# Optimization experiments

Measured on AMD Instinct MI355X. Metric: run time of the kernel, lower is better.

Reference implementation:

```python
import jax, jax.numpy as jnp
import numpy as np

D = 256; H = 8; DFFN = 512; L = 3; P = 4
SHAPES = [(64, 64), (32, 32), (16, 16)]  # (Hl, Wl) per level
LQ = 64 * 64
LV = sum(h * w for h, w in SHAPES)
B = 1


def _ln(x, g, b):
    m = x.mean(-1, keepdims=True)
    v = ((x - m) ** 2).mean(-1, keepdims=True)
    return (x - m) / jnp.sqrt(v + 1e-5) * g + b


def _mha(q, k, v, Wi, bi, Wo, bo):
    Dh = D // H
    B_, Lq, _ = q.shape
    qp = (q @ Wi[:D].T + bi[:D]).reshape(B_, Lq, H, Dh)
    kp = (k @ Wi[D:2 * D].T + bi[D:2 * D]).reshape(B_, -1, H, Dh)
    vp = (v @ Wi[2 * D:].T + bi[2 * D:]).reshape(B_, -1, H, Dh)
    s = jnp.einsum('bqhd,bkhd->bhqk', qp, kp) / jnp.sqrt(jnp.asarray(Dh, qp.dtype))
    a = jax.nn.softmax(s, axis=-1)
    o = jnp.einsum('bhqk,bkhd->bqhd', a, vp).reshape(B_, Lq, D)
    return o @ Wo.T + bo


def _msdeform(q, ref, value_in, off_w, off_b, attn_w, attn_b, val_w, val_b, out_w, out_b):
    B_, Lq, _ = q.shape
    Dh = D // H
    value = (value_in @ val_w.T + val_b).reshape(B_, LV, H, Dh)
    off = (q @ off_w.T + off_b).reshape(B_, Lq, H, L, P, 2)
    aw = jax.nn.softmax((q @ attn_w.T + attn_b).reshape(B_, Lq, H, L * P), axis=-1)
    aw = aw.reshape(B_, Lq, H, L, P)
    norm = jnp.asarray([[w, h] for h, w in SHAPES], dtype=q.dtype)  # (W,H) per level
    loc = ref[:, :, None, :, None, :] + off / norm[None, None, None, :, None, :]
    out = jnp.zeros((B_, H, Lq, Dh), q.dtype)
    start = 0
    for l, (Hl, Wl) in enumerate(SHAPES):
        v = value[:, start:start + Hl * Wl].transpose(0, 2, 1, 3)  # [B,H,Hl*Wl,Dh]
        start += Hl * Wl
        # grid_sample align_corners=False, padding_mode='zeros'
        x = loc[:, :, :, l, :, 0] * Wl - 0.5  # [B,Lq,H,P]
        y = loc[:, :, :, l, :, 1] * Hl - 0.5
        x0 = jnp.floor(x); y0 = jnp.floor(y)
        wx = x - x0; wy = y - y0
        x0i = x0.astype(jnp.int32); y0i = y0.astype(jnp.int32)

        def gather(xi, yi):
            valid = ((xi >= 0) & (xi < Wl) & (yi >= 0) & (yi < Hl)).astype(q.dtype)
            idx = jnp.clip(yi, 0, Hl - 1) * Wl + jnp.clip(xi, 0, Wl - 1)
            idx = idx.transpose(0, 2, 1, 3).reshape(B_, H, Lq * P, 1)
            g = jnp.take_along_axis(v, idx, axis=2)  # [B,H,Lq*P,Dh]
            return g * valid.transpose(0, 2, 1, 3).reshape(B_, H, Lq * P, 1)

        g00 = gather(x0i, y0i); g01 = gather(x0i + 1, y0i)
        g10 = gather(x0i, y0i + 1); g11 = gather(x0i + 1, y0i + 1)

        def r(t):
            return t.transpose(0, 2, 1, 3).reshape(B_, H, Lq * P, 1)

        wxr = r(wx); wyr = r(wy)
        samp = (g00 * (1 - wxr) * (1 - wyr) + g01 * wxr * (1 - wyr)
                + g10 * (1 - wxr) * wyr + g11 * wxr * wyr)
        a = r(aw[:, :, :, l])
        out = out + (samp * a).reshape(B_, H, Lq, P, Dh).sum(axis=3)
    o = out.transpose(0, 2, 1, 3).reshape(B_, Lq, D)
    return o @ out_w.T + out_b


def _forward(bev_queries, img_feats_flat, ref_points, bev_pos,
             mha_in_w, mha_in_b, mha_out_w, mha_out_b, norm1_g, norm1_b,
             off_w, off_b, attn_w, attn_b, val_w, val_b, ca_out_w, ca_out_b,
             norm2_g, norm2_b, ffn_w1, ffn_b1, ffn_w2, ffn_b2, ffn_g, ffn_bb):
    q = bev_queries + bev_pos
    x = _ln(bev_queries + _mha(q, q, bev_queries, mha_in_w, mha_in_b, mha_out_w, mha_out_b),
            norm1_g, norm1_b)
    q2 = x + bev_pos
    x = _ln(x + _msdeform(q2, ref_points, img_feats_flat, off_w, off_b, attn_w, attn_b,
                          val_w, val_b, ca_out_w, ca_out_b), norm2_g, norm2_b)
    h = jax.nn.relu(x @ ffn_w1.T + ffn_b1) @ ffn_w2.T + ffn_b2
    return _ln(x + h, ffn_g, ffn_bb)


def setup_inputs() -> dict:
    key = jax.random.key(0)
    ks = jax.random.split(key, 16)
    f = jax.random.normal
    return {
        'bev_queries': f(ks[0], (B, LQ, D), jnp.float32),
        'img_feats_flat': f(ks[1], (B, LV, D), jnp.float32),
        'ref_points': jax.random.uniform(ks[2], (B, LQ, L, 2), jnp.float32),
        'spatial_shapes': jnp.asarray(SHAPES, dtype=jnp.int32),
        'bev_pos': f(ks[3], (B, LQ, D), jnp.float32),
        'mha_in_w': f(ks[4], (3 * D, D)) * 0.02, 'mha_in_b': jnp.zeros((3 * D,)),
        'mha_out_w': f(ks[5], (D, D)) * 0.02, 'mha_out_b': jnp.zeros((D,)),
        'norm1_g': jnp.ones((D,)), 'norm1_b': jnp.zeros((D,)),
        'off_w': f(ks[6], (H * L * P * 2, D)) * 0.02,
        'off_b': jax.random.uniform(ks[7], (H * L * P * 2,), minval=-2.0, maxval=2.0),
        'attn_w': f(ks[8], (H * L * P, D)) * 0.02, 'attn_b': jnp.zeros((H * L * P,)),
        'val_w': f(ks[9], (D, D)) * 0.02, 'val_b': jnp.zeros((D,)),
        'ca_out_w': f(ks[10], (D, D)) * 0.02, 'ca_out_b': jnp.zeros((D,)),
        'norm2_g': jnp.ones((D,)), 'norm2_b': jnp.zeros((D,)),
        'ffn_w1': f(ks[11], (DFFN, D)) * 0.02, 'ffn_b1': jnp.zeros((DFFN,)),
        'ffn_w2': f(ks[12], (D, DFFN)) * 0.02, 'ffn_b2': jnp.zeros((D,)),
        'ffn_g': jnp.ones((D,)), 'ffn_bb': jnp.zeros((D,)),
    }


def reference(bev_queries, img_feats_flat, ref_points, spatial_shapes, bev_pos,
              mha_in_w, mha_in_b, mha_out_w, mha_out_b, norm1_g, norm1_b,
              off_w, off_b, attn_w, attn_b, val_w, val_b, ca_out_w, ca_out_b,
              norm2_g, norm2_b, ffn_w1, ffn_b1, ffn_w2, ffn_b2, ffn_g, ffn_bb):
    del spatial_shapes  # static; baked into SHAPES
    return _forward(bev_queries, img_feats_flat, ref_points, bev_pos,
                    mha_in_w, mha_in_b, mha_out_w, mha_out_b, norm1_g, norm1_b,
                    off_w, off_b, attn_w, attn_b, val_w, val_b, ca_out_w, ca_out_b,
                    norm2_g, norm2_b, ffn_w1, ffn_b1, ffn_w2, ffn_b2, ffn_g, ffn_bb)
```

## Files before the change

kernel.cpp:

```cpp
#include <hip/hip_runtime.h>
#include <math.h>


#define LQ_N 4096
#define LV_N 5376

typedef short short8 __attribute__((ext_vector_type(8)));
typedef float f32x4 __attribute__((ext_vector_type(4)));

__device__ inline unsigned short f2b(float f) {
  union { float f; unsigned u; } v;
  v.f = f;
  return (unsigned short)((v.u + 0x7FFFu + ((v.u >> 16) & 1u)) >> 16);
}

__device__ __forceinline__ void gemm_body(
    const float* __restrict__ A, const float* __restrict__ A2,
    const float* __restrict__ W, const float* __restrict__ bias,
    float* __restrict__ C, int M, int N, int K, int relu, int bm, int bn) {
  __shared__ unsigned short Asb[64][40];
  __shared__ unsigned short Wsb[64][40];
  const int tid = threadIdx.x;
  const int w = tid >> 6, lane = tid & 63;
  const int g = lane >> 4, li = lane & 15;
  f32x4 acc[4] = {{0.f, 0.f, 0.f, 0.f}, {0.f, 0.f, 0.f, 0.f},
                  {0.f, 0.f, 0.f, 0.f}, {0.f, 0.f, 0.f, 0.f}};
  for (int k0 = 0; k0 < K; k0 += 32) {
    __syncthreads();
#pragma unroll
    for (int i = 0; i < 2; ++i) {
      int r = (tid >> 3) + i * 32;
      int c = (tid & 7) * 4;
      int gr = bm + r;
      float4 av = make_float4(0.f, 0.f, 0.f, 0.f);
      if (gr < M) {
        av = *reinterpret_cast<const float4*>(&A[(size_t)gr * K + k0 + c]);
        if (A2) {
          float4 bv = *reinterpret_cast<const float4*>(&A2[(size_t)gr * K + k0 + c]);
          av.x += bv.x; av.y += bv.y; av.z += bv.z; av.w += bv.w;
        }
      }
      Asb[r][c + 0] = f2b(av.x); Asb[r][c + 1] = f2b(av.y);
      Asb[r][c + 2] = f2b(av.z); Asb[r][c + 3] = f2b(av.w);
      int gw = bn + r;
      float4 wv = make_float4(0.f, 0.f, 0.f, 0.f);
      if (gw < N) wv = *reinterpret_cast<const float4*>(&W[(size_t)gw * K + k0 + c]);
      Wsb[r][c + 0] = f2b(wv.x); Wsb[r][c + 1] = f2b(wv.y);
      Wsb[r][c + 2] = f2b(wv.z); Wsb[r][c + 3] = f2b(wv.w);
    }
    __syncthreads();
    short8 af = *reinterpret_cast<const short8*>(&Asb[w * 16 + li][g * 8]);
#pragma unroll
    for (int nt = 0; nt < 4; ++nt) {
      short8 wf = *reinterpret_cast<const short8*>(&Wsb[nt * 16 + li][g * 8]);
      acc[nt] = __builtin_amdgcn_mfma_f32_16x16x32_bf16(af, wf, acc[nt], 0, 0, 0);
    }
  }
#pragma unroll
  for (int nt = 0; nt < 4; ++nt) {
#pragma unroll
    for (int reg = 0; reg < 4; ++reg) {
      int row = bm + w * 16 + g * 4 + reg;
      int col = bn + nt * 16 + li;
      if (row < M && col < N) {
        float v = acc[nt][reg] + bias[col];
        if (relu) v = fmaxf(v, 0.f);
        C[(size_t)row * N + col] = v;
      }
    }
  }
}

__global__ __launch_bounds__(256) void gemm_bf16_kernel(
    const float* __restrict__ A, const float* __restrict__ A2,
    const float* __restrict__ W, const float* __restrict__ bias,
    float* __restrict__ C, int M, int N, int K, int relu) {
  gemm_body(A, A2, W, bias, C, M, N, K, relu, blockIdx.y * 64, blockIdx.x * 64);
}

__global__ __launch_bounds__(256) void qkv_kernel(
    const float* __restrict__ bevq, const float* __restrict__ bevpos,
    const float* __restrict__ w, const float* __restrict__ b,
    float* __restrict__ out) {
  const int z = blockIdx.z;
  gemm_body(bevq, z < 2 ? bevpos : nullptr, w + (size_t)z * 256 * 256, b + z * 256,
            out + (size_t)z * 1048576, LQ_N, 256, 256, 0,
            blockIdx.y * 64, blockIdx.x * 64);
}

__global__ __launch_bounds__(256) void attn_mfma_kernel(
    const float* __restrict__ qp, const float* __restrict__ kp,
    const float* __restrict__ vp, float* __restrict__ out) {
  const int h = blockIdx.y;
  const int q0 = blockIdx.x * 64;
  __shared__ unsigned short Qsb[64][40];
  __shared__ unsigned short Ksb[64][40];
  __shared__ unsigned short Vtb[32][72];
  __shared__ unsigned short Plds[4][16][72];
  const int tid = threadIdx.x;
  const int w = tid >> 6, lane = tid & 63;
  const int g = lane >> 4, li = lane & 15;
  const float scale = 0.17677669529663687f;

#pragma unroll
  for (int i = 0; i < 2; ++i) {
    int r = (tid >> 3) + i * 32;
    int c = (tid & 7) * 4;
    float4 v = *reinterpret_cast<const float4*>(&qp[(size_t)(q0 + r) * 256 + h * 32 + c]);
    Qsb[r][c + 0] = f2b(v.x * scale); Qsb[r][c + 1] = f2b(v.y * scale);
    Qsb[r][c + 2] = f2b(v.z * scale); Qsb[r][c + 3] = f2b(v.w * scale);
  }
  __syncthreads();
  short8 qfrag = *reinterpret_cast<const short8*>(&Qsb[w * 16 + li][g * 8]);

  f32x4 oacc[2] = {{0.f, 0.f, 0.f, 0.f}, {0.f, 0.f, 0.f, 0.f}};
  float m_run[4] = {-1e30f, -1e30f, -1e30f, -1e30f};
  float l_run[4] = {0.f, 0.f, 0.f, 0.f};

  for (int kt = 0; kt < LQ_N; kt += 64) {
    __syncthreads();
#pragma unroll
    for (int i = 0; i < 2; ++i) {
      int r = (tid >> 3) + i * 32;
      int c = (tid & 7) * 4;
      float4 kv = *reinterpret_cast<const float4*>(&kp[(size_t)(kt + r) * 256 + h * 32 + c]);
      Ksb[r][c + 0] = f2b(kv.x); Ksb[r][c + 1] = f2b(kv.y);
      Ksb[r][c + 2] = f2b(kv.z); Ksb[r][c + 3] = f2b(kv.w);
      float4 vv = *reinterpret_cast<const float4*>(&vp[(size_t)(kt + r) * 256 + h * 32 + c]);
      Vtb[c + 0][r] = f2b(vv.x); Vtb[c + 1][r] = f2b(vv.y);
      Vtb[c + 2][r] = f2b(vv.z); Vtb[c + 3][r] = f2b(vv.w);
    }
    __syncthreads();

    f32x4 s[4];
#pragma unroll
    for (int nt = 0; nt < 4; ++nt) {
      short8 kf = *reinterpret_cast<const short8*>(&Ksb[nt * 16 + li][g * 8]);
      f32x4 z = {0.f, 0.f, 0.f, 0.f};
      s[nt] = __builtin_amdgcn_mfma_f32_16x16x32_bf16(qfrag, kf, z, 0, 0, 0);
    }

#pragma unroll
    for (int reg = 0; reg < 4; ++reg) {
      float m = fmaxf(fmaxf(s[0][reg], s[1][reg]), fmaxf(s[2][reg], s[3][reg]));
      m = fmaxf(m, __shfl_xor(m, 1));
      m = fmaxf(m, __shfl_xor(m, 2));
      m = fmaxf(m, __shfl_xor(m, 4));
      m = fmaxf(m, __shfl_xor(m, 8));
      float mn = fmaxf(m_run[reg], m);
      float corr = __expf(m_run[reg] - mn);
      m_run[reg] = mn;
      float ls = 0.f;
#pragma unroll
      for (int nt = 0; nt < 4; ++nt) {
        float p = __expf(s[nt][reg] - mn);
        s[nt][reg] = p;
        ls += p;
      }
      ls += __shfl_xor(ls, 1);
      ls += __shfl_xor(ls, 2);
      ls += __shfl_xor(ls, 4);
      ls += __shfl_xor(ls, 8);
      l_run[reg] = l_run[reg] * corr + ls;
#pragma unroll
      for (int nt = 0; nt < 4; ++nt)
        Plds[w][g * 4 + reg][nt * 16 + li] = f2b(s[nt][reg]);
      oacc[0][reg] *= corr;
      oacc[1][reg] *= corr;
    }

#pragma unroll
    for (int ks = 0; ks < 2; ++ks) {
      short8 pf = *reinterpret_cast<const short8*>(&Plds[w][li][ks * 32 + g * 8]);
#pragma unroll
      for (int nt2 = 0; nt2 < 2; ++nt2) {
        short8 vf = *reinterpret_cast<const short8*>(&Vtb[nt2 * 16 + li][ks * 32 + g * 8]);
        oacc[nt2] = __builtin_amdgcn_mfma_f32_16x16x32_bf16(pf, vf, oacc[nt2], 0, 0, 0);
      }
    }
  }

#pragma unroll
  for (int reg = 0; reg < 4; ++reg) {
    float invl = 1.f / l_run[reg];
    int row = q0 + w * 16 + g * 4 + reg;
#pragma unroll
    for (int nt2 = 0; nt2 < 2; ++nt2)
      out[(size_t)row * 256 + h * 32 + nt2 * 16 + li] = oacc[nt2][reg] * invl;
  }
}

__global__ __launch_bounds__(256) void add_ln_kernel(
    const float* __restrict__ a, const float* __restrict__ b,
    const float* __restrict__ g, const float* __restrict__ bb,
    float* __restrict__ out) {
  int row = blockIdx.x, t = threadIdx.x;
  float v = a[(size_t)row * 256 + t] + b[(size_t)row * 256 + t];
  float s = v;
#pragma unroll
  for (int m = 32; m >= 1; m >>= 1) s += __shfl_xor(s, m);
  __shared__ float red[4], red2[4];
  int wave = t >> 6, lane = t & 63;
  if (lane == 0) red[wave] = s;
  __syncthreads();
  float mean = (red[0] + red[1] + red[2] + red[3]) * (1.f / 256.f);
  float dv = v - mean;
  float s2 = dv * dv;
#pragma unroll
  for (int m = 32; m >= 1; m >>= 1) s2 += __shfl_xor(s2, m);
  if (lane == 0) red2[wave] = s2;
  __syncthreads();
  float var = (red2[0] + red2[1] + red2[2] + red2[3]) * (1.f / 256.f);
  out[(size_t)row * 256 + t] = dv * rsqrtf(var + 1e-5f) * g[t] + bb[t];
}

__global__ __launch_bounds__(256) void msdeform_kernel(
    const float* __restrict__ value,
    const float* __restrict__ off,
    const float* __restrict__ awl,
    const float* __restrict__ ref,
    float* __restrict__ out) {
  int qi = blockIdx.x;
  int tid = threadIdx.x;
  int h = tid >> 5, d = tid & 31;
  float w[12];
  float mx = -1e30f;
#pragma unroll
  for (int j = 0; j < 12; ++j) {
    w[j] = awl[(size_t)qi * 96 + h * 12 + j];
    mx = fmaxf(mx, w[j]);
  }
  float ssum = 0.f;
#pragma unroll
  for (int j = 0; j < 12; ++j) {
    w[j] = __expf(w[j] - mx);
    ssum += w[j];
  }
  float inv = 1.f / ssum;
  const int starts[3] = {0, 4096, 5120};
  const int dims[3] = {64, 32, 16};
  float acc = 0.f;
#pragma unroll
  for (int l = 0; l < 3; ++l) {
    const int Wl = dims[l], Hl = dims[l];
    float rx = ref[(size_t)qi * 6 + l * 2 + 0];
    float ry = ref[(size_t)qi * 6 + l * 2 + 1];
    auto fetch = [&](int xi, int yi) -> float {
      if (xi < 0 || xi >= Wl || yi < 0 || yi >= Hl) return 0.f;
      return value[(size_t)(starts[l] + yi * Wl + xi) * 256 + h * 32 + d];
    };
#pragma unroll
    for (int p = 0; p < 4; ++p) {
      int oidx = qi * 192 + ((h * 3 + l) * 4 + p) * 2;
      float ox = off[oidx], oy = off[oidx + 1];
      float x = (rx + ox / (float)Wl) * (float)Wl - 0.5f;
      float y = (ry + oy / (float)Hl) * (float)Hl - 0.5f;
      float x0f = floorf(x), y0f = floorf(y);
      float wx = x - x0f, wy = y - y0f;
      int x0 = (int)x0f, y0 = (int)y0f;
      float g00 = fetch(x0, y0);
      float g01 = fetch(x0 + 1, y0);
      float g10 = fetch(x0, y0 + 1);
      float g11 = fetch(x0 + 1, y0 + 1);
      float samp = g00 * (1.f - wx) * (1.f - wy) + g01 * wx * (1.f - wy) +
                   g10 * (1.f - wx) * wy + g11 * wx * wy;
      acc += samp * w[l * 4 + p] * inv;
    }
  }
  out[(size_t)qi * 256 + h * 32 + d] = acc;
}

extern "C" void kernel_launch(void* const* d_in, const int* in_sizes, int n_in,
                              void* d_out, int out_size, void* d_ws, size_t ws_size,
                              hipStream_t stream) {
  const float* bevq   = (const float*)d_in[0];
  const float* img    = (const float*)d_in[1];
  const float* refp   = (const float*)d_in[2];
  const float* bevpos = (const float*)d_in[4];
  const float* mha_in_w  = (const float*)d_in[5];
  const float* mha_in_b  = (const float*)d_in[6];
  const float* mha_out_w = (const float*)d_in[7];
  const float* mha_out_b = (const float*)d_in[8];
  const float* norm1_g = (const float*)d_in[9];
  const float* norm1_b = (const float*)d_in[10];
  const float* off_w  = (const float*)d_in[11];
  const float* off_b  = (const float*)d_in[12];
  const float* attn_w = (const float*)d_in[13];
  const float* attn_b = (const float*)d_in[14];
  const float* val_w  = (const float*)d_in[15];
  const float* val_b  = (const float*)d_in[16];
  const float* ca_out_w = (const float*)d_in[17];
  const float* ca_out_b = (const float*)d_in[18];
  const float* norm2_g = (const float*)d_in[19];
  const float* norm2_b = (const float*)d_in[20];
  const float* ffn_w1 = (const float*)d_in[21];
  const float* ffn_b1 = (const float*)d_in[22];
  const float* ffn_w2 = (const float*)d_in[23];
  const float* ffn_b2 = (const float*)d_in[24];
  const float* ffn_g  = (const float*)d_in[25];
  const float* ffn_bb = (const float*)d_in[26];

  float* ws = (float*)d_ws;
  const size_t M1 = 1048576;
  float* bufQP  = ws + 1 * M1;
  float* bufKP  = ws + 2 * M1;
  float* bufVP  = ws + 3 * M1;
  float* bufAO  = ws + 4 * M1;
  float* bufX   = ws + 5 * M1;
  float* bufX2  = ws + 6 * M1;
  float* bufH1  = ws + 7 * M1;
  float* bufVAL = ws + 9 * M1;
  float* bufY   = ws;

  float* out = (float*)d_out;

  dim3 blk(256);
  qkv_kernel<<<dim3(4, 64, 3), blk, 0, stream>>>(bevq, bevpos, mha_in_w, mha_in_b, bufQP);
  attn_mfma_kernel<<<dim3(64, 8), blk, 0, stream>>>(bufQP, bufKP, bufVP, bufAO);
  gemm_bf16_kernel<<<dim3(4, 64), blk, 0, stream>>>(bufAO, nullptr, mha_out_w, mha_out_b,
                                                    bufY, LQ_N, 256, 256, 0);
  add_ln_kernel<<<dim3(4096), blk, 0, stream>>>(bevq, bufY, norm1_g, norm1_b, bufX);
  gemm_bf16_kernel<<<dim3(4, 84), blk, 0, stream>>>(img, nullptr, val_w, val_b,
                                                    bufVAL, LV_N, 256, 256, 0);
  gemm_bf16_kernel<<<dim3(3, 64), blk, 0, stream>>>(bufX, bevpos, off_w, off_b,
                                                    bufQP, LQ_N, 192, 256, 0);
  gemm_bf16_kernel<<<dim3(2, 64), blk, 0, stream>>>(bufX, bevpos, attn_w, attn_b,
                                                    bufKP, LQ_N, 96, 256, 0);
  msdeform_kernel<<<dim3(4096), blk, 0, stream>>>(bufVAL, bufQP, bufKP, refp, bufAO);
  gemm_bf16_kernel<<<dim3(4, 64), blk, 0, stream>>>(bufAO, nullptr, ca_out_w, ca_out_b,
                                                    bufY, LQ_N, 256, 256, 0);
  add_ln_kernel<<<dim3(4096), blk, 0, stream>>>(bufX, bufY, norm2_g, norm2_b, bufX2);
  gemm_bf16_kernel<<<dim3(8, 64), blk, 0, stream>>>(bufX2, nullptr, ffn_w1, ffn_b1,
                                                    bufH1, LQ_N, 512, 256, 1);
  gemm_bf16_kernel<<<dim3(4, 64), blk, 0, stream>>>(bufH1, nullptr, ffn_w2, ffn_b2,
                                                    bufY, LQ_N, 256, 512, 0);
  add_ln_kernel<<<dim3(4096), blk, 0, stream>>>(bufX2, bufY, ffn_g, ffn_bb, out);

  (void)in_sizes; (void)n_in; (void)out_size; (void)ws_size;
}
```

Baseline: 485.7 us.

## Emit bf16 Q/K/V from QKV GEMM and stream K/V-transposed directly in attention

The QKV projection now writes bf16 outputs, with the softmax scale folded into Q, instead of fp32. A new transpose kernel lays V out head-major for the PV MFMA. The attention kernel loads Q, K and V fragments directly from global memory rather than staging them through LDS with barriers, processes 128 keys per iteration, swizzles the P tile in LDS and raises wave priority around MFMA sections. This removes per-tile fp32-to-bf16 conversion, halves K/V bandwidth and drops block-wide syncs, at the cost of uncoalesced direct global fragment loads and an extra transpose launch.

```diff
diff --git a/kernel.cpp b/kernel.cpp
--- a/kernel.cpp
+++ b/kernel.cpp
@@ -17,7 +17,8 @@
 __device__ __forceinline__ void gemm_body(
     const float* __restrict__ A, const float* __restrict__ A2,
     const float* __restrict__ W, const float* __restrict__ bias,
-    float* __restrict__ C, int M, int N, int K, int relu, int bm, int bn) {
+    void* __restrict__ C, int M, int N, int K, int mode, float oscale,
+    int bm, int bn) {
   __shared__ unsigned short Asb[64][40];
   __shared__ unsigned short Wsb[64][40];
   const int tid = threadIdx.x;
@@ -64,8 +65,11 @@
       int col = bn + nt * 16 + li;
       if (row < M && col < N) {
         float v = acc[nt][reg] + bias[col];
-        if (relu) v = fmaxf(v, 0.f);
-        C[(size_t)row * N + col] = v;
+        if (mode == 1) v = fmaxf(v, 0.f);
+        if (mode == 2)
+          ((unsigned short*)C)[(size_t)row * N + col] = f2b(v * oscale);
+        else
+          ((float*)C)[(size_t)row * N + col] = v;
       }
     }
   }
@@ -75,74 +79,90 @@
     const float* __restrict__ A, const float* __restrict__ A2,
     const float* __restrict__ W, const float* __restrict__ bias,
     float* __restrict__ C, int M, int N, int K, int relu) {
-  gemm_body(A, A2, W, bias, C, M, N, K, relu, blockIdx.y * 64, blockIdx.x * 64);
+  gemm_body(A, A2, W, bias, C, M, N, K, relu, 1.f,
+            blockIdx.y * 64, blockIdx.x * 64);
 }
 
 __global__ __launch_bounds__(256) void qkv_kernel(
     const float* __restrict__ bevq, const float* __restrict__ bevpos,
     const float* __restrict__ w, const float* __restrict__ b,
-    float* __restrict__ out) {
+    unsigned short* __restrict__ out) {
   const int z = blockIdx.z;
+  float sc = (z == 0) ? 0.17677669529663687f : 1.0f;
   gemm_body(bevq, z < 2 ? bevpos : nullptr, w + (size_t)z * 256 * 256, b + z * 256,
-            out + (size_t)z * 1048576, LQ_N, 256, 256, 0,
+            out + (size_t)z * 1048576, LQ_N, 256, 256, 2, sc,
             blockIdx.y * 64, blockIdx.x * 64);
 }
 
+__global__ __launch_bounds__(256) void transpose_bf16_kernel(
+    const unsigned short* __restrict__ in, unsigned short* __restrict__ out) {
+  __shared__ unsigned short t[64][72];
+  const int tid = threadIdx.x;
+  const int bx = blockIdx.x;
+  const int by = blockIdx.y;
+#pragma unroll
+  for (int i = 0; i < 2; ++i) {
+    int r = (tid >> 3) + i * 32;
+    int c = (tid & 7) * 8;
+    short8 v = *reinterpret_cast<const short8*>(
+        &in[(size_t)(bx * 64 + r) * 256 + by * 64 + c]);
+#pragma unroll
+    for (int j = 0; j < 8; ++j) {
+      int A = c + j;
+      int f = (A ^ (A >> 3)) & 7;
+      t[A][r ^ (f << 3)] = (unsigned short)v[j];
+    }
+  }
+  __syncthreads();
+#pragma unroll
+  for (int i = 0; i < 2; ++i) {
+    int r2 = (tid >> 3) + i * 32;
+    int c2 = (tid & 7) * 8;
+    int f = (r2 ^ (r2 >> 3)) & 7;
+    short8 v = *reinterpret_cast<const short8*>(&t[r2][c2 ^ (f << 3)]);
+    *reinterpret_cast<short8*>(
+        &out[(size_t)(by * 64 + r2) * 4096 + bx * 64 + c2]) = v;
+  }
+}
+
 __global__ __launch_bounds__(256) void attn_mfma_kernel(
-    const float* __restrict__ qp, const float* __restrict__ kp,
-    const float* __restrict__ vp, float* __restrict__ out) {
+    const unsigned short* __restrict__ qb, const unsigned short* __restrict__ kb,
+    const unsigned short* __restrict__ vt, float* __restrict__ out) {
   const int h = blockIdx.y;
   const int q0 = blockIdx.x * 64;
-  __shared__ unsigned short Qsb[64][40];
-  __shared__ unsigned short Ksb[64][40];
-  __shared__ unsigned short Vtb[32][72];
-  __shared__ unsigned short Plds[4][16][72];
+  __shared__ unsigned short Plds[4][16][136];
   const int tid = threadIdx.x;
   const int w = tid >> 6, lane = tid & 63;
   const int g = lane >> 4, li = lane & 15;
-  const float scale = 0.17677669529663687f;
-
-#pragma unroll
-  for (int i = 0; i < 2; ++i) {
-    int r = (tid >> 3) + i * 32;
-    int c = (tid & 7) * 4;
-    float4 v = *reinterpret_cast<const float4*>(&qp[(size_t)(q0 + r) * 256 + h * 32 + c]);
-    Qsb[r][c + 0] = f2b(v.x * scale); Qsb[r][c + 1] = f2b(v.y * scale);
-    Qsb[r][c + 2] = f2b(v.z * scale); Qsb[r][c + 3] = f2b(v.w * scale);
-  }
-  __syncthreads();
-  short8 qfrag = *reinterpret_cast<const short8*>(&Qsb[w * 16 + li][g * 8]);
+
+  short8 qfrag = *reinterpret_cast<const short8*>(
+      &qb[(size_t)(q0 + w * 16 + li) * 256 + h * 32 + g * 8]);
 
   f32x4 oacc[2] = {{0.f, 0.f, 0.f, 0.f}, {0.f, 0.f, 0.f, 0.f}};
   float m_run[4] = {-1e30f, -1e30f, -1e30f, -1e30f};
   float l_run[4] = {0.f, 0.f, 0.f, 0.f};
 
-  for (int kt = 0; kt < LQ_N; kt += 64) {
-    __syncthreads();
-#pragma unroll
-    for (int i = 0; i < 2; ++i) {
-      int r = (tid >> 3) + i * 32;
-      int c = (tid & 7) * 4;
-      float4 kv = *reinterpret_cast<const float4*>(&kp[(size_t)(kt + r) * 256 + h * 32 + c]);
-      Ksb[r][c + 0] = f2b(kv.x); Ksb[r][c + 1] = f2b(kv.y);
-      Ksb[r][c + 2] = f2b(kv.z); Ksb[r][c + 3] = f2b(kv.w);
-      float4 vv = *reinterpret_cast<const float4*>(&vp[(size_t)(kt + r) * 256 + h * 32 + c]);
-      Vtb[c + 0][r] = f2b(vv.x); Vtb[c + 1][r] = f2b(vv.y);
-      Vtb[c + 2][r] = f2b(vv.z); Vtb[c + 3][r] = f2b(vv.w);
-    }
-    __syncthreads();
-
-    f32x4 s[4];
-#pragma unroll
-    for (int nt = 0; nt < 4; ++nt) {
-      short8 kf = *reinterpret_cast<const short8*>(&Ksb[nt * 16 + li][g * 8]);
+  const unsigned short* kbase = kb + h * 32 + g * 8;
+  const unsigned short* vbase = vt + (size_t)(h * 32) * 4096;
+  const int pswz = (li & 7) << 3;
+
+  for (int kt = 0; kt < LQ_N; kt += 128) {
+    f32x4 s[8];
+    __builtin_amdgcn_s_setprio(1);
+#pragma unroll
+    for (int nt = 0; nt < 8; ++nt) {
+      short8 kf = *reinterpret_cast<const short8*>(
+          &kbase[(size_t)(kt + nt * 16 + li) * 256]);
       f32x4 z = {0.f, 0.f, 0.f, 0.f};
       s[nt] = __builtin_amdgcn_mfma_f32_16x16x32_bf16(qfrag, kf, z, 0, 0, 0);
     }
+    __builtin_amdgcn_s_setprio(0);
 
 #pragma unroll
     for (int reg = 0; reg < 4; ++reg) {
-      float m = fmaxf(fmaxf(s[0][reg], s[1][reg]), fmaxf(s[2][reg], s[3][reg]));
+      float m = s[0][reg];
+#pragma unroll
+      for (int nt = 1; nt < 8; ++nt) m = fmaxf(m, s[nt][reg]);
       m = fmaxf(m, __shfl_xor(m, 1));
       m = fmaxf(m, __shfl_xor(m, 2));
       m = fmaxf(m, __shfl_xor(m, 4));
@@ -151,33 +171,36 @@
       float corr = __expf(m_run[reg] - mn);
       m_run[reg] = mn;
       float ls = 0.f;
-#pragma unroll
-      for (int nt = 0; nt < 4; ++nt) {
+      int qr = g * 4 + reg;
+      int swz = (qr & 7) << 3;
+#pragma unroll
+      for (int nt = 0; nt < 8; ++nt) {
         float p = __expf(s[nt][reg] - mn);
-        s[nt][reg] = p;
         ls += p;
+        Plds[w][qr][(nt * 16 + li) ^ swz] = f2b(p);
       }
       ls += __shfl_xor(ls, 1);
       ls += __shfl_xor(ls, 2);
       ls += __shfl_xor(ls, 4);
       ls += __shfl_xor(ls, 8);
       l_run[reg] = l_run[reg] * corr + ls;
-#pragma unroll
-      for (int nt = 0; nt < 4; ++nt)
-        Plds[w][g * 4 + reg][nt * 16 + li] = f2b(s[nt][reg]);
       oacc[0][reg] *= corr;
       oacc[1][reg] *= corr;
     }
 
-#pragma unroll
-    for (int ks = 0; ks < 2; ++ks) {
-      short8 pf = *reinterpret_cast<const short8*>(&Plds[w][li][ks * 32 + g * 8]);
+    __builtin_amdgcn_s_setprio(1);
+#pragma unroll
+    for (int ks = 0; ks < 4; ++ks) {
+      short8 pf = *reinterpret_cast<const short8*>(
+          &Plds[w][li][(ks * 32 + g * 8) ^ pswz]);
 #pragma unroll
       for (int nt2 = 0; nt2 < 2; ++nt2) {
-        short8 vf = *reinterpret_cast<const short8*>(&Vtb[nt2 * 16 + li][ks * 32 + g * 8]);
+        short8 vf = *reinterpret_cast<const short8*>(
+            &vbase[(size_t)(nt2 * 16 + li) * 4096 + kt + ks * 32 + g * 8]);
         oacc[nt2] = __builtin_amdgcn_mfma_f32_16x16x32_bf16(pf, vf, oacc[nt2], 0, 0, 0);
       }
     }
+    __builtin_amdgcn_s_setprio(0);
   }
 
 #pragma unroll
@@ -302,31 +325,34 @@
 
   float* ws = (float*)d_ws;
   const size_t M1 = 1048576;
-  float* bufQP  = ws + 1 * M1;
-  float* bufKP  = ws + 2 * M1;
-  float* bufVP  = ws + 3 * M1;
+  float* bufY   = ws;
+  unsigned short* qkb = (unsigned short*)(ws + 1 * M1);
+  unsigned short* vb  = (unsigned short*)(ws + 2 * M1);
+  float* bufOFF = ws + 3 * M1;
   float* bufAO  = ws + 4 * M1;
   float* bufX   = ws + 5 * M1;
   float* bufX2  = ws + 6 * M1;
   float* bufH1  = ws + 7 * M1;
   float* bufVAL = ws + 9 * M1;
-  float* bufY   = ws;
+  float* bufAWL = ws;
 
   float* out = (float*)d_out;
 
   dim3 blk(256);
-  qkv_kernel<<<dim3(4, 64, 3), blk, 0, stream>>>(bevq, bevpos, mha_in_w, mha_in_b, bufQP);
-  attn_mfma_kernel<<<dim3(64, 8), blk, 0, stream>>>(bufQP, bufKP, bufVP, bufAO);
+  qkv_kernel<<<dim3(4, 64, 3), blk, 0, stream>>>(bevq, bevpos, mha_in_w, mha_in_b, qkb);
+  transpose_bf16_kernel<<<dim3(64, 4), blk, 0, stream>>>(vb, vb + 1048576);
+  attn_mfma_kernel<<<dim3(64, 8), blk, 0, stream>>>(qkb, qkb + 1048576,
+                                                    vb + 1048576, bufAO);
   gemm_bf16_kernel<<<dim3(4, 64), blk, 0, stream>>>(bufAO, nullptr, mha_out_w, mha_out_b,
                                                     bufY, LQ_N, 256, 256, 0);
   add_ln_kernel<<<dim3(4096), blk, 0, stream>>>(bevq, bufY, norm1_g, norm1_b, bufX);
   gemm_bf16_kernel<<<dim3(4, 84), blk, 0, stream>>>(img, nullptr, val_w, val_b,
                                                     bufVAL, LV_N, 256, 256, 0);
   gemm_bf16_kernel<<<dim3(3, 64), blk, 0, stream>>>(bufX, bevpos, off_w, off_b,
-                                                    bufQP, LQ_N, 192, 256, 0);
+                                                    bufOFF, LQ_N, 192, 256, 0);
   gemm_bf16_kernel<<<dim3(2, 64), blk, 0, stream>>>(bufX, bevpos, attn_w, attn_b,
-                                                    bufKP, LQ_N, 96, 256, 0);
-  msdeform_kernel<<<dim3(4096), blk, 0, stream>>>(bufVAL, bufQP, bufKP, refp, bufAO);
+                                                    bufAWL, LQ_N, 96, 256, 0);
+  msdeform_kernel<<<dim3(4096), blk, 0, stream>>>(bufVAL, bufOFF, bufAWL, refp, bufAO);
   gemm_bf16_kernel<<<dim3(4, 64), blk, 0, stream>>>(bufAO, nullptr, ca_out_w, ca_out_b,
                                                     bufY, LQ_N, 256, 256, 0);
   add_ln_kernel<<<dim3(4096), blk, 0, stream>>>(bufX, bufY, norm2_g, norm2_b, bufX2);
```

New measurement: 428.7 us. 11.7% less time.
